# Kernel tuning notes

Measured on AMD Instinct MI355X. Metric: run time of the kernel, lower is better.

## Reference

```python
import jax, jax.numpy as jnp
import numpy as np

Bsz, Hs, Ws, D = 16, 48, 48, 768
N, R, NITERS = 64, 4, 12
NR = N * R


def setup_inputs() -> dict:
    key = jax.random.key(0)
    ks = jax.random.split(key, 16)
    w = lambda k, shape, s=0.02: jax.random.normal(k, shape, jnp.float32) * s
    return {
        "x": jax.random.normal(ks[0], (Bsz, Hs, Ws, D), jnp.float32),
        "W_B": w(ks[1], (D, NR)), "b_B": jnp.zeros((NR,), jnp.float32),
        "W_C": w(ks[2], (D, NR)), "b_C": jnp.zeros((NR,), jnp.float32),
        "W_X": w(ks[3], (D, R)), "b_X": jnp.zeros((R,), jnp.float32),
        "W_dec": w(ks[4], (D, N)), "b_dec": jnp.zeros((N,), jnp.float32),
        "W_th": w(ks[5], (D, N // 2)), "b_th": jnp.zeros((N // 2,), jnp.float32),
        "W_lam": w(ks[6], (D, 1)), "b_lam": jnp.zeros((1,), jnp.float32),
        "B_bias": jnp.ones((NR,), jnp.float32),
        "C_bias": jnp.ones((NR,), jnp.float32),
        "conv_w": w(ks[7], (3, 3, 1, N), 0.1),  # HWIO, depthwise (groups=N)
        "conv_b": jnp.zeros((N,), jnp.float32),
        "W_out": w(ks[8], (NR, D)), "b_out": jnp.zeros((D,), jnp.float32),
    }


def _rope(v, th):
    # v: [B,R,H,W,N], th: [B,H,W,N/2] (broadcast over R). Interleaved pairs.
    c = jnp.cos(th)[:, None]
    s = jnp.sin(th)[:, None]
    vr = v.reshape(v.shape[:-1] + (v.shape[-1] // 2, 2))
    v1, v2 = vr[..., 0], vr[..., 1]
    return jnp.stack([v1 * c - v2 * s, v1 * s + v2 * c], axis=-1).reshape(v.shape)


def reference(x, W_B, b_B, W_C, b_C, W_X, b_X, W_dec, b_dec, W_th, b_th,
              W_lam, b_lam, B_bias, C_bias, conv_w, conv_b, W_out, b_out):
    silu = jax.nn.silu
    Bb, Hh, Ww = x.shape[0], x.shape[1], x.shape[2]

    # Input-dependent (iteration-invariant) projections
    B_proj = silu(x @ W_B + b_B + B_bias).reshape(Bb, Hh, Ww, N, R)
    C_proj = silu(x @ W_C + b_C + C_bias).reshape(Bb, Hh, Ww, N, R)
    B_base = jnp.transpose(B_proj, (0, 4, 1, 2, 3))  # [B,R,H,W,N]
    C_base = jnp.transpose(C_proj, (0, 4, 1, 2, 3))
    Xb = jnp.transpose(silu(x @ W_X + b_X), (0, 3, 1, 2))[..., None]  # [B,R,H,W,1]
    alpha = jax.nn.sigmoid(x @ W_dec + b_dec)[:, None]  # [B,1,H,W,N]
    theta = x @ W_th + b_th                              # [B,H,W,N/2]
    gamma = jax.nn.sigmoid(x @ W_lam + b_lam)[:, None]  # [B,1,H,W,1]

    def diffuse(Hst):
        hf = Hst.reshape(Bb * R, Hh, Ww, N)
        y = jax.lax.conv_general_dilated(
            hf, conv_w, (1, 1), 'SAME',
            dimension_numbers=('NHWC', 'HWIO', 'NHWC'),
            feature_group_count=N) + conv_b
        return y.reshape(Bb, R, Hh, Ww, N)

    Hst = jnp.zeros((Bb, R, Hh, Ww, N), x.dtype)
    prev = None
    for i in range(NITERS):
        inj = _rope(B_base, theta * (i + 1)) * Xb
        Hst = diffuse(Hst)
        if prev is None:
            Hst = alpha * Hst + inj
        else:
            Hst = alpha * Hst + (1.0 - gamma) * alpha * prev + gamma * inj
        prev = inj

    C_rot = _rope(C_base, theta * NITERS)  # layer_idx = n_iters-1 -> scale n_iters
    Hg = C_rot * Hst                        # [B,R,H,W,N]
    Ho = jnp.transpose(Hg, (0, 2, 3, 1, 4)).reshape(Bb, Hh, Ww, R * N)
    return silu(Ho @ W_out + b_out)
```

## Files before the change

kernel.cpp:

```cpp
#include <hip/hip_runtime.h>
#include <hip/hip_bf16.h>
#include <math.h>

#define PTOT 36864
#define DIM 768
#define NCOLS 640
#define IMG 2304
#define KSTEPS 24
#define NPBLK 288

typedef unsigned short ushort_t;
typedef unsigned int uint_t;
typedef __attribute__((ext_vector_type(8))) short bfx8;
typedef __attribute__((ext_vector_type(4))) float f32x4;

#define MFMA_BF16(a, b, c) __builtin_amdgcn_mfma_f32_16x16x32_bf16((a), (b), (c), 0, 0, 0)

__device__ __forceinline__ float sigmoidf_(float v) { return 1.f / (1.f + __expf(-v)); }
__device__ __forceinline__ float siluf_(float v)    { return v   / (1.f + __expf(-v)); }
__device__ __forceinline__ float rfl(float v) {
  return __int_as_float(__builtin_amdgcn_readfirstlane(__float_as_int(v)));
}
__device__ __forceinline__ float bf2f(ushort_t h) {
  return __uint_as_float(((uint_t)h) << 16);
}

typedef __attribute__((address_space(3))) unsigned int lds_uint;
typedef __attribute__((address_space(1))) const unsigned int g_uint;
__device__ __forceinline__ void glds16(const void* gsrc, void* ldst) {
  __builtin_amdgcn_global_load_lds((g_uint*)gsrc, (lds_uint*)ldst, 16, 0, 0);
}

__device__ __forceinline__ void split2(float a, float b, uint_t& hw, uint_t& lw) {
  __hip_bfloat162 hh = __float22bfloat162_rn(make_float2(a, b));
  uint_t hu; __builtin_memcpy(&hu, &hh, 4);
  float ha = __uint_as_float(hu << 16);
  float hb = __uint_as_float(hu & 0xffff0000u);
  __hip_bfloat162 ll = __float22bfloat162_rn(make_float2(a - ha, b - hb));
  uint_t lu; __builtin_memcpy(&lu, &ll, 4);
  hw = hu; lw = lu;
}
__device__ __forceinline__ uint_t cvt2_hi(float a, float b) {
  __hip_bfloat162 hh = __float22bfloat162_rn(make_float2(a, b));
  uint_t hu; __builtin_memcpy(&hu, &hh, 4);
  return hu;
}
__device__ __forceinline__ ushort_t f2bf(float a) {
  return (ushort_t)(cvt2_hi(a, 0.f) & 0xffffu);
}
__device__ __forceinline__ void split8_fast(const float* f, uint4& hi, uint4& lo) {
  uint_t* Hp = (uint_t*)&hi;
  uint_t* Lp = (uint_t*)&lo;
#pragma unroll
  for (int q = 0; q < 4; ++q) split2(f[2 * q], f[2 * q + 1], Hp[q], Lp[q]);
}
__device__ __forceinline__ void cvt8_hi(const float* f, uint4& hi) {
  uint_t* Hp = (uint_t*)&hi;
#pragma unroll
  for (int q = 0; q < 4; ++q) Hp[q] = cvt2_hi(f[2 * q], f[2 * q + 1]);
}

__global__ void pack_kernel(
    const float* __restrict__ W_B, const float* __restrict__ W_C,
    const float* __restrict__ W_dec, const float* __restrict__ W_th,
    const float* __restrict__ W_X, const float* __restrict__ W_lam,
    const float* __restrict__ b_B, const float* __restrict__ b_C,
    const float* __restrict__ b_dec, const float* __restrict__ b_th,
    const float* __restrict__ b_X, const float* __restrict__ b_lam,
    const float* __restrict__ B_bias, const float* __restrict__ C_bias,
    const float* __restrict__ W_out,
    ushort_t* __restrict__ WhiT, ushort_t* __restrict__ WloT,
    ushort_t* __restrict__ WoT, float* __restrict__ bias_all) {
  int idx = blockIdx.x * 256 + threadIdx.x;
  const int NW = NCOLS * DIM;
  const int NWO = DIM * 256;
  if (idx < NW) {
    int c = idx / DIM, k = idx - c * DIM;
    float v;
    if      (c < 256) v = W_B[k * 256 + c];
    else if (c < 512) v = W_C[k * 256 + (c - 256)];
    else if (c < 576) v = W_dec[k * 64 + (c - 512)];
    else if (c < 608) v = W_th[k * 32 + (c - 576)];
    else if (c < 612) v = W_X[k * 4 + (c - 608)];
    else if (c == 612) v = W_lam[k];
    else v = 0.f;
    uint_t hw, lw;
    split2(v, 0.f, hw, lw);
    WhiT[idx] = (ushort_t)(hw & 0xffffu);
    WloT[idx] = (ushort_t)(lw & 0xffffu);
  } else if (idx < NW + NWO) {
    int t = idx - NW;
    int j = t / 256, k = t - j * 256;
    WoT[t] = f2bf(W_out[k * DIM + j]);
  }
  if (idx < NCOLS) {
    int c = idx;
    float v;
    if      (c < 256) v = b_B[c] + B_bias[c];
    else if (c < 512) v = b_C[c - 256] + C_bias[c - 256];
    else if (c < 576) v = b_dec[c - 512];
    else if (c < 608) v = b_th[c - 576];
    else if (c < 612) v = b_X[c - 608];
    else if (c == 612) v = b_lam[0];
    else v = 0.f;
    bias_all[c] = v;
  }
}

template <int HEAVY>
__global__ __launch_bounds__(512, HEAVY ? 4 : 6) void gemm_proj_glds(
    const float* __restrict__ x, const ushort_t* __restrict__ WhiT,
    const ushort_t* __restrict__ WloT, const float* __restrict__ biasall,
    ushort_t* __restrict__ projBC, float* __restrict__ projS) {
  __shared__ ushort_t Ash[2][4096];
  __shared__ ushort_t Asl[HEAVY ? 2 : 1][HEAVY ? 4096 : 4];
  __shared__ float    Bsf[2][4096];
  const int tid = threadIdx.x;
  const int lane = tid & 63, wv = tid >> 6;
  const int wr = wv >> 2, wc = wv & 3;
  const int lk = lane >> 4, lm = lane & 15;

  int cblk, pblk;
  if (HEAVY) {
    int lin = blockIdx.x;
    int id2 = (lin & 7) * 36 + (lin >> 3);
    cblk = 4; pblk = id2;
  } else {
    int lin = blockIdx.x;
    int id2 = (lin & 7) * 144 + (lin >> 3);
    cblk = id2 & 3; pblk = id2 >> 2;
  }
  const int c0 = cblk * 128, p0 = pblk * 128;

  f32x4 acc[4][2];
#pragma unroll
  for (int i = 0; i < 4; ++i)
#pragma unroll
    for (int j = 0; j < 2; ++j) acc[i][j] = (f32x4)0.f;

  auto stage = [&](int buf, int kidx) {
    const int k0 = kidx * 32;
    {
      int mb = __builtin_amdgcn_readfirstlane(wv * 64);
      int m = mb + lane;
      int row = m >> 2, sp = m & 3;
      int g = sp ^ ((row >> 1) & 3);
      glds16(&WhiT[(size_t)(c0 + row) * DIM + k0 + g * 8],
             (void*)&Ash[buf][mb * 8]);
    }
    if (HEAVY) {
      int mb = __builtin_amdgcn_readfirstlane(wv * 64);
      int m = mb + lane;
      int row = m >> 2, sp = m & 3;
      int g = sp ^ ((row >> 1) & 3);
      glds16(&WloT[(size_t)(c0 + row) * DIM + k0 + g * 8],
             (void*)&Asl[buf][mb * 8]);
    }
#pragma unroll
    for (int j = 0; j < 2; ++j) {
      int mb = __builtin_amdgcn_readfirstlane(j * 512 + wv * 64);
      int m = mb + lane;
      int row = m >> 3, sp = m & 7;
      int g = sp ^ (row & 7);
      glds16(&x[(size_t)(p0 + row) * DIM + k0 + g * 4],
             (void*)&Bsf[buf][mb * 4]);
    }
  };

  stage(0, 0);
  __syncthreads();

  for (int kidx = 0; kidx < KSTEPS; ++kidx) {
    const int cur = kidx & 1;
    if (kidx + 1 < KSTEPS) stage(cur ^ 1, kidx + 1);

    bfx8 ah[4], al[4];
#pragma unroll
    for (int f = 0; f < 4; ++f) {
      int row = wr * 64 + f * 16 + lm;
      int sp = lk ^ ((row >> 1) & 3);
      int idx = (row * 4 + sp) * 8;
      ah[f] = *(const bfx8*)&Ash[cur][idx];
      if (HEAVY) al[f] = *(const bfx8*)&Asl[cur][idx];
    }
    bfx8 bh[2], bl[2];
#pragma unroll
    for (int n = 0; n < 2; ++n) {
      int row = wc * 32 + n * 16 + lm;
      int sp0 = (2 * lk)     ^ (row & 7);
      int sp1 = (2 * lk + 1) ^ (row & 7);
      float fv[8];
      *(float4*)&fv[0] = *(const float4*)&Bsf[cur][(row * 8 + sp0) * 4];
      *(float4*)&fv[4] = *(const float4*)&Bsf[cur][(row * 8 + sp1) * 4];
      if (HEAVY) {
        uint4 hv, lv;
        split8_fast(fv, hv, lv);
        bh[n] = *(bfx8*)&hv;
        bl[n] = *(bfx8*)&lv;
      } else {
        uint4 hv;
        cvt8_hi(fv, hv);
        bh[n] = *(bfx8*)&hv;
      }
    }
#pragma unroll
    for (int i = 0; i < 4; ++i)
#pragma unroll
      for (int j = 0; j < 2; ++j) {
        acc[i][j] = MFMA_BF16(ah[i], bh[j], acc[i][j]);
        if (HEAVY) {
          acc[i][j] = MFMA_BF16(al[i], bh[j], acc[i][j]);
          acc[i][j] = MFMA_BF16(ah[i], bl[j], acc[i][j]);
        }
      }
    __syncthreads();
  }

#pragma unroll
  for (int i = 0; i < 4; ++i) {
#pragma unroll
    for (int r = 0; r < 4; ++r) {
      int c = c0 + wr * 64 + i * 16 + lk * 4 + r;
      float bia = biasall[c];
      if (HEAVY) {
        if (c >= 613) continue;
        int rowo = c - 512;
        bool do_silu = (c >= 608 && c < 612);
        bool do_sig  = (c < 576) || (c == 612);
#pragma unroll
        for (int j = 0; j < 2; ++j) {
          float z = acc[i][j][r] + bia;
          if (do_silu) z = siluf_(z);
          else if (do_sig) z = sigmoidf_(z);
          projS[(size_t)rowo * PTOT + p0 + wc * 32 + j * 16 + lm] = z;
        }
      } else {
#pragma unroll
        for (int j = 0; j < 2; ++j) {
          float z = siluf_(acc[i][j][r] + bia);
          projBC[(size_t)c * PTOT + p0 + wc * 32 + j * 16 + lm] = f2bf(z);
        }
      }
    }
  }
}

__global__ __launch_bounds__(256) void iter_kernel(
    const ushort_t* __restrict__ projBC, const float* __restrict__ projS,
    const float* __restrict__ conv_w, const float* __restrict__ conv_b,
    ushort_t* __restrict__ HgBf) {
  const int n2 = blockIdx.x;
  const int r  = blockIdx.y;
  const int b  = blockIdx.z;
  const int n0 = 2 * n2, n1 = n0 + 1;
  const int tid = threadIdx.x;
  const int bh = tid >> 4, bw = tid & 15;
  const int pbase = b * IMG;

  __shared__ float2 HS[2][50 * 51];

  float w0[9], w1[9];
#pragma unroll
  for (int t = 0; t < 9; ++t) {
    w0[t] = rfl(conv_w[t * 64 + n0]);
    w1[t] = rfl(conv_w[t * 64 + n1]);
  }
  const float cvb0 = rfl(conv_b[n0]), cvb1 = rfl(conv_b[n1]);

  {
    float4 zz = {0.f, 0.f, 0.f, 0.f};
    float4* z = (float4*)&HS[0][0];
#pragma unroll
    for (int u = 0; u < 10; ++u) {
      int q = tid + 256 * u;
      if (q < 2550) z[q] = zz;
    }
  }

  const ushort_t* rowB0 = projBC + (size_t)(n0 * 4 + r) * PTOT + pbase;
  const ushort_t* rowB1 = projBC + (size_t)(n1 * 4 + r) * PTOT + pbase;
  const ushort_t* rowC0 = projBC + (size_t)(256 + n0 * 4 + r) * PTOT + pbase;
  const ushort_t* rowC1 = projBC + (size_t)(256 + n1 * 4 + r) * PTOT + pbase;
  const float* rowA0 = projS + (size_t)n0 * PTOT + pbase;
  const float* rowA1 = projS + (size_t)n1 * PTOT + pbase;
  const float* rowTh = projS + (size_t)(64 + n2) * PTOT + pbase;
  const float* rowXv = projS + (size_t)(96 + r) * PTOT + pbase;
  const float* rowGm = projS + (size_t)100 * PTOT + pbase;

  float be0[9], be1[9], cb[9], sb[9], al0[9], al1[9], gmv[9];
#pragma unroll
  for (int s = 0; s < 9; ++s) {
    int dy = s / 3, dx = s - 3 * dy;
    int i = (3 * bh + dy) * 48 + 3 * bw + dx;
    float sn, cn;
    __sincosf(rowTh[i], &sn, &cn);
    cb[s] = cn; sb[s] = sn;
    float B0 = bf2f(rowB0[i]), B1 = bf2f(rowB1[i]), X = rowXv[i];
    be0[s] = (B0 * cn - B1 * sn) * X;
    be1[s] = (B0 * sn + B1 * cn) * X;
    al0[s] = rowA0[i]; al1[s] = rowA1[i];
    gmv[s] = rowGm[i];
  }
  __syncthreads();

  int cur = 0;
  for (int it = 0; it < 12; ++it) {
    float a0[9], a1[9];
#pragma unroll
    for (int s = 0; s < 9; ++s) { a0[s] = cvb0; a1[s] = cvb1; }
#pragma unroll
    for (int yy = 0; yy < 5; ++yy) {
      float2 row[5];
#pragma unroll
      for (int xx = 0; xx < 5; ++xx)
        row[xx] = HS[cur][(3 * bh + yy) * 51 + 3 * bw + xx];
#pragma unroll
      for (int dy = 0; dy < 3; ++dy) {
        int ty = yy - dy;
        if (ty < 0 || ty > 2) continue;
#pragma unroll
        for (int dx = 0; dx < 3; ++dx)
#pragma unroll
          for (int tx = 0; tx < 3; ++tx) {
            a0[dy * 3 + dx] += row[dx + tx].x * w0[ty * 3 + tx];
            a1[dy * 3 + dx] += row[dx + tx].y * w1[ty * 3 + tx];
          }
      }
    }
#pragma unroll
    for (int s = 0; s < 9; ++s) {
      int dy = s / 3, dx = s - 3 * dy;
      float h0, h1;
      if (it == 0) {
        h0 = al0[s] * a0[s] + be0[s];
        h1 = al1[s] * a1[s] + be1[s];
      } else {
        float p0 = be0[s] * cb[s] + be1[s] * sb[s];
        float p1 = be1[s] * cb[s] - be0[s] * sb[s];
        float g = gmv[s];
        h0 = al0[s] * (a0[s] + (1.f - g) * p0) + g * be0[s];
        h1 = al1[s] * (a1[s] + (1.f - g) * p1) + g * be1[s];
      }
      float2 hw; hw.x = h0; hw.y = h1;
      HS[cur ^ 1][(3 * bh + dy + 1) * 51 + (3 * bw + dx + 1)] = hw;
      if (it < 11) {
        float nb0 = be0[s] * cb[s] - be1[s] * sb[s];
        float nb1 = be0[s] * sb[s] + be1[s] * cb[s];
        be0[s] = nb0; be1[s] = nb1;
      }
    }
    __syncthreads();
    cur ^= 1;
  }

  ushort_t* outRow0 = HgBf + (size_t)(r * 64 + n0) * PTOT + pbase;
  ushort_t* outRow1 = HgBf + (size_t)(r * 64 + n1) * PTOT + pbase;
#pragma unroll
  for (int s = 0; s < 9; ++s) {
    int dy = s / 3, dx = s - 3 * dy;
    int i = (3 * bh + dy) * 48 + 3 * bw + dx;
    float c2 = cb[s] * cb[s] - sb[s] * sb[s], s2 = 2.f * cb[s] * sb[s];
    float c4 = c2 * c2 - s2 * s2,             s4 = 2.f * c2 * s2;
    float c8 = c4 * c4 - s4 * s4,             s8 = 2.f * c4 * s4;
    float c12 = c8 * c4 - s8 * s4,            s12 = c8 * s4 + s8 * c4;
    float C0 = bf2f(rowC0[i]), C1 = bf2f(rowC1[i]);
    float cr0 = C0 * c12 - C1 * s12;
    float cr1 = C0 * s12 + C1 * c12;
    float2 hv = HS[cur][(3 * bh + dy + 1) * 51 + (3 * bw + dx + 1)];
    outRow0[i] = f2bf(cr0 * hv.x);
    outRow1[i] = f2bf(cr1 * hv.y);
  }
}

__global__ __launch_bounds__(256) void transpose_cvt(
    const ushort_t* __restrict__ HgBf, ushort_t* __restrict__ Hbf) {
  __shared__ float T[64][65];
  const int tid = threadIdx.x;
  const int p0 = blockIdx.x * 64;
  const int k0 = blockIdx.y * 64;
  {
    int row = tid >> 2, q = tid & 3;
    const ushort_t* src = &HgBf[(size_t)(k0 + row) * PTOT + p0 + q * 16];
    uint4 u0 = *(const uint4*)src;
    uint4 u1 = *(const uint4*)(src + 8);
    const uint_t* up = (const uint_t*)&u0;
#pragma unroll
    for (int t = 0; t < 4; ++t) {
      T[row][q * 16 + 2 * t]     = bf2f((ushort_t)(up[t] & 0xffffu));
      T[row][q * 16 + 2 * t + 1] = bf2f((ushort_t)(up[t] >> 16));
    }
    const uint_t* vp = (const uint_t*)&u1;
#pragma unroll
    for (int t = 0; t < 4; ++t) {
      T[row][q * 16 + 8 + 2 * t]     = bf2f((ushort_t)(vp[t] & 0xffffu));
      T[row][q * 16 + 8 + 2 * t + 1] = bf2f((ushort_t)(vp[t] >> 16));
    }
  }
  __syncthreads();
  {
    int pr = tid >> 2, kq = tid & 3;
    uint_t Hw[8];
#pragma unroll
    for (int q = 0; q < 8; ++q)
      Hw[q] = cvt2_hi(T[kq * 16 + 2 * q][pr], T[kq * 16 + 2 * q + 1][pr]);
    size_t off = (size_t)(p0 + pr) * 256 + k0 + kq * 16;
    *(uint4*)&Hbf[off]     = make_uint4(Hw[0], Hw[1], Hw[2], Hw[3]);
    *(uint4*)&Hbf[off + 8] = make_uint4(Hw[4], Hw[5], Hw[6], Hw[7]);
  }
}

__global__ __launch_bounds__(512, 6) void gemm_out_glds(
    const ushort_t* __restrict__ Hbf, const ushort_t* __restrict__ WoT,
    const float* __restrict__ b_out, float* __restrict__ out) {
  __shared__ ushort_t As[2][4096];
  __shared__ ushort_t Bs[2][4096];
  const int tid = threadIdx.x;
  const int lane = tid & 63, wv = tid >> 6;
  const int wr = wv >> 2, wc = wv & 3;
  const int lk = lane >> 4, lm = lane & 15;
  int lin = blockIdx.x;
  int id2 = (lin & 7) * 216 + (lin >> 3);
  const int jblk = id2 % 6, pblk = id2 / 6;
  const int j0 = jblk * 128, p0 = pblk * 128;

  f32x4 acc[4][2];
#pragma unroll
  for (int i = 0; i < 4; ++i)
#pragma unroll
    for (int j = 0; j < 2; ++j) acc[i][j] = (f32x4)0.f;

  auto stage = [&](int buf, int kidx) {
    const int k0 = kidx * 32;
    {
      int mb = __builtin_amdgcn_readfirstlane(wv * 64);
      int m = mb + lane;
      int row = m >> 2, sp = m & 3;
      int g = sp ^ ((row >> 1) & 3);
      glds16(&Hbf[(size_t)(p0 + row) * 256 + k0 + g * 8],
             (void*)&As[buf][mb * 8]);
    }
    {
      int mb = __builtin_amdgcn_readfirstlane(wv * 64);
      int m = mb + lane;
      int row = m >> 2, sp = m & 3;
      int g = sp ^ ((row >> 1) & 3);
      glds16(&WoT[(size_t)(j0 + row) * 256 + k0 + g * 8],
             (void*)&Bs[buf][mb * 8]);
    }
  };

  stage(0, 0);
  __syncthreads();

  for (int kidx = 0; kidx < 8; ++kidx) {
    const int cur = kidx & 1;
    if (kidx + 1 < 8) stage(cur ^ 1, kidx + 1);
    bfx8 ah[4], bh[2];
#pragma unroll
    for (int f = 0; f < 4; ++f) {
      int ra = wr * 64 + f * 16 + lm;
      int sa = lk ^ ((ra >> 1) & 3);
      ah[f] = *(const bfx8*)&As[cur][(ra * 4 + sa) * 8];
    }
#pragma unroll
    for (int n = 0; n < 2; ++n) {
      int rb = wc * 32 + n * 16 + lm;
      int sb2 = lk ^ ((rb >> 1) & 3);
      bh[n] = *(const bfx8*)&Bs[cur][(rb * 4 + sb2) * 8];
    }
#pragma unroll
    for (int i = 0; i < 4; ++i)
#pragma unroll
      for (int j = 0; j < 2; ++j)
        acc[i][j] = MFMA_BF16(ah[i], bh[j], acc[i][j]);
    __syncthreads();
  }

  float bo[2];
#pragma unroll
  for (int jj = 0; jj < 2; ++jj) bo[jj] = b_out[j0 + wc * 32 + jj * 16 + lm];
#pragma unroll
  for (int i = 0; i < 4; ++i) {
#pragma unroll
    for (int r = 0; r < 4; ++r) {
      int p = p0 + wr * 64 + i * 16 + lk * 4 + r;
      size_t rowoff = (size_t)p * DIM;
#pragma unroll
      for (int jj = 0; jj < 2; ++jj) {
        out[rowoff + j0 + wc * 32 + jj * 16 + lm] =
            siluf_(acc[i][jj][r] + bo[jj]);
      }
    }
  }
}

extern "C" void kernel_launch(void* const* d_in, const int* in_sizes, int n_in,
                              void* d_out, int out_size, void* d_ws, size_t ws_size,
                              hipStream_t stream) {
  const float* x      = (const float*)d_in[0];
  const float* W_B    = (const float*)d_in[1];
  const float* b_B    = (const float*)d_in[2];
  const float* W_C    = (const float*)d_in[3];
  const float* b_C    = (const float*)d_in[4];
  const float* W_X    = (const float*)d_in[5];
  const float* b_X    = (const float*)d_in[6];
  const float* W_dec  = (const float*)d_in[7];
  const float* b_dec  = (const float*)d_in[8];
  const float* W_th   = (const float*)d_in[9];
  const float* b_th   = (const float*)d_in[10];
  const float* W_lam  = (const float*)d_in[11];
  const float* b_lam  = (const float*)d_in[12];
  const float* B_bias = (const float*)d_in[13];
  const float* C_bias = (const float*)d_in[14];
  const float* conv_w = (const float*)d_in[15];
  const float* conv_b = (const float*)d_in[16];
  const float* W_out  = (const float*)d_in[17];
  const float* b_out  = (const float*)d_in[18];
  float* out = (float*)d_out;

  ushort_t* WhiT   = (ushort_t*)d_ws;
  ushort_t* WloT   = WhiT + (size_t)NCOLS * DIM;
  ushort_t* WoT    = WloT + (size_t)NCOLS * DIM;
  float* bias_all  = (float*)(WoT + (size_t)DIM * 256);
  ushort_t* projBC = (ushort_t*)(bias_all + NCOLS);
  float* projS     = (float*)(projBC + (size_t)512 * PTOT);
  ushort_t* HgBf   = (ushort_t*)(projS + (size_t)104 * PTOT);
  ushort_t* Hbf    = HgBf + (size_t)256 * PTOT;

  const int pack_elems = NCOLS * DIM + DIM * 256;
  pack_kernel<<<(pack_elems + 255) / 256, 256, 0, stream>>>(
      W_B, W_C, W_dec, W_th, W_X, W_lam,
      b_B, b_C, b_dec, b_th, b_X, b_lam, B_bias, C_bias, W_out,
      WhiT, WloT, WoT, bias_all);

  gemm_proj_glds<0><<<dim3(4 * NPBLK), 512, 0, stream>>>(
      x, WhiT, WloT, bias_all, projBC, projS);
  gemm_proj_glds<1><<<dim3(NPBLK), 512, 0, stream>>>(
      x, WhiT, WloT, bias_all, projBC, projS);

  iter_kernel<<<dim3(32, 4, 16), 256, 0, stream>>>(
      projBC, projS, conv_w, conv_b, HgBf);

  transpose_cvt<<<dim3(PTOT / 64, 4), 256, 0, stream>>>(HgBf, Hbf);

  gemm_out_glds<<<dim3(6 * NPBLK), 512, 0, stream>>>(
      Hbf, WoT, b_out, out);
}
```

Measured before the change: 244.1 us.

## Load GEMM operands directly from global memory into registers, bypassing LDS

The light projection GEMM (B/C columns) and the output GEMM drop LDS double-buffering and barriers. Each wave now loads its MFMA fragments straight from global memory into registers. The heavy split-precision projection path is split into its own non-templated kernel and keeps its LDS staging. This removes LDS traffic and __syncthreads, but gives up operand sharing across waves, so global/L2 traffic rises and there is no software prefetch to hide load latency.

Result: slower. 440.5 us (+80.5%).

```diff
diff --git a/kernel.cpp b/kernel.cpp
--- a/kernel.cpp
+++ b/kernel.cpp
@@ -107,29 +107,82 @@
   }
 }
 
-template <int HEAVY>
-__global__ __launch_bounds__(512, HEAVY ? 4 : 6) void gemm_proj_glds(
+__global__ __launch_bounds__(512, 6) void gemm_proj_direct(
+    const float* __restrict__ x, const ushort_t* __restrict__ WhiT,
+    const float* __restrict__ biasall, ushort_t* __restrict__ projBC) {
+  const int tid = threadIdx.x;
+  const int lane = tid & 63, wv = tid >> 6;
+  const int wr = wv >> 2, wc = wv & 3;
+  const int lk = lane >> 4, lm = lane & 15;
+
+  int lin = blockIdx.x;
+  int id2 = (lin & 7) * 144 + (lin >> 3);
+  const int cblk = id2 & 3, pblk = id2 >> 2;
+  const int c0 = cblk * 128, p0 = pblk * 128;
+
+  const ushort_t* wbase = WhiT + (size_t)(c0 + wr * 64 + lm) * DIM + lk * 8;
+  const float*    xbase = x    + (size_t)(p0 + wc * 32 + lm) * DIM + lk * 8;
+
+  f32x4 acc[4][2];
+#pragma unroll
+  for (int i = 0; i < 4; ++i)
+#pragma unroll
+    for (int j = 0; j < 2; ++j) acc[i][j] = (f32x4)0.f;
+
+  for (int kidx = 0; kidx < KSTEPS; ++kidx) {
+    const int k0 = kidx * 32;
+    bfx8 ah[4];
+#pragma unroll
+    for (int f = 0; f < 4; ++f)
+      ah[f] = *(const bfx8*)(wbase + (size_t)f * 16 * DIM + k0);
+    bfx8 bh[2];
+#pragma unroll
+    for (int n = 0; n < 2; ++n) {
+      const float* xq = xbase + (size_t)n * 16 * DIM + k0;
+      float fv[8];
+      *(float4*)&fv[0] = *(const float4*)xq;
+      *(float4*)&fv[4] = *(const float4*)(xq + 4);
+      uint4 hv;
+      cvt8_hi(fv, hv);
+      bh[n] = *(bfx8*)&hv;
+    }
+#pragma unroll
+    for (int i = 0; i < 4; ++i)
+#pragma unroll
+      for (int j = 0; j < 2; ++j)
+        acc[i][j] = MFMA_BF16(ah[i], bh[j], acc[i][j]);
+  }
+
+#pragma unroll
+  for (int i = 0; i < 4; ++i) {
+#pragma unroll
+    for (int r = 0; r < 4; ++r) {
+      int c = c0 + wr * 64 + i * 16 + lk * 4 + r;
+      float bia = biasall[c];
+#pragma unroll
+      for (int j = 0; j < 2; ++j) {
+        float z = siluf_(acc[i][j][r] + bia);
+        projBC[(size_t)c * PTOT + p0 + wc * 32 + j * 16 + lm] = f2bf(z);
+      }
+    }
+  }
+}
+
+__global__ __launch_bounds__(512, 4) void gemm_proj_heavy(
     const float* __restrict__ x, const ushort_t* __restrict__ WhiT,
     const ushort_t* __restrict__ WloT, const float* __restrict__ biasall,
-    ushort_t* __restrict__ projBC, float* __restrict__ projS) {
+    float* __restrict__ projS) {
   __shared__ ushort_t Ash[2][4096];
-  __shared__ ushort_t Asl[HEAVY ? 2 : 1][HEAVY ? 4096 : 4];
+  __shared__ ushort_t Asl[2][4096];
   __shared__ float    Bsf[2][4096];
   const int tid = threadIdx.x;
   const int lane = tid & 63, wv = tid >> 6;
   const int wr = wv >> 2, wc = wv & 3;
   const int lk = lane >> 4, lm = lane & 15;
 
-  int cblk, pblk;
-  if (HEAVY) {
-    int lin = blockIdx.x;
-    int id2 = (lin & 7) * 36 + (lin >> 3);
-    cblk = 4; pblk = id2;
-  } else {
-    int lin = blockIdx.x;
-    int id2 = (lin & 7) * 144 + (lin >> 3);
-    cblk = id2 & 3; pblk = id2 >> 2;
-  }
+  int lin = blockIdx.x;
+  int id2 = (lin & 7) * 36 + (lin >> 3);
+  const int cblk = 4, pblk = id2;
   const int c0 = cblk * 128, p0 = pblk * 128;
 
   f32x4 acc[4][2];
@@ -148,7 +201,7 @@
       glds16(&WhiT[(size_t)(c0 + row) * DIM + k0 + g * 8],
              (void*)&Ash[buf][mb * 8]);
     }
-    if (HEAVY) {
+    {
       int mb = __builtin_amdgcn_readfirstlane(wv * 64);
       int m = mb + lane;
       int row = m >> 2, sp = m & 3;
@@ -181,7 +234,7 @@
       int sp = lk ^ ((row >> 1) & 3);
       int idx = (row * 4 + sp) * 8;
       ah[f] = *(const bfx8*)&Ash[cur][idx];
-      if (HEAVY) al[f] = *(const bfx8*)&Asl[cur][idx];
+      al[f] = *(const bfx8*)&Asl[cur][idx];
     }
     bfx8 bh[2], bl[2];
 #pragma unroll
@@ -192,26 +245,18 @@
       float fv[8];
       *(float4*)&fv[0] = *(const float4*)&Bsf[cur][(row * 8 + sp0) * 4];
       *(float4*)&fv[4] = *(const float4*)&Bsf[cur][(row * 8 + sp1) * 4];
-      if (HEAVY) {
-        uint4 hv, lv;
-        split8_fast(fv, hv, lv);
-        bh[n] = *(bfx8*)&hv;
-        bl[n] = *(bfx8*)&lv;
-      } else {
-        uint4 hv;
-        cvt8_hi(fv, hv);
-        bh[n] = *(bfx8*)&hv;
-      }
+      uint4 hv, lv;
+      split8_fast(fv, hv, lv);
+      bh[n] = *(bfx8*)&hv;
+      bl[n] = *(bfx8*)&lv;
     }
 #pragma unroll
     for (int i = 0; i < 4; ++i)
 #pragma unroll
       for (int j = 0; j < 2; ++j) {
         acc[i][j] = MFMA_BF16(ah[i], bh[j], acc[i][j]);
-        if (HEAVY) {
-          acc[i][j] = MFMA_BF16(al[i], bh[j], acc[i][j]);
-          acc[i][j] = MFMA_BF16(ah[i], bl[j], acc[i][j]);
-        }
+        acc[i][j] = MFMA_BF16(al[i], bh[j], acc[i][j]);
+        acc[i][j] = MFMA_BF16(ah[i], bl[j], acc[i][j]);
       }
     __syncthreads();
   }
@@ -221,25 +266,17 @@
 #pragma unroll
     for (int r = 0; r < 4; ++r) {
       int c = c0 + wr * 64 + i * 16 + lk * 4 + r;
+      if (c >= 613) continue;
       float bia = biasall[c];
-      if (HEAVY) {
-        if (c >= 613) continue;
-        int rowo = c - 512;
-        bool do_silu = (c >= 608 && c < 612);
-        bool do_sig  = (c < 576) || (c == 612);
-#pragma unroll
-        for (int j = 0; j < 2; ++j) {
-          float z = acc[i][j][r] + bia;
-          if (do_silu) z = siluf_(z);
-          else if (do_sig) z = sigmoidf_(z);
-          projS[(size_t)rowo * PTOT + p0 + wc * 32 + j * 16 + lm] = z;
-        }
-      } else {
-#pragma unroll
-        for (int j = 0; j < 2; ++j) {
-          float z = siluf_(acc[i][j][r] + bia);
-          projBC[(size_t)c * PTOT + p0 + wc * 32 + j * 16 + lm] = f2bf(z);
-        }
+      int rowo = c - 512;
+      bool do_silu = (c >= 608 && c < 612);
+      bool do_sig  = (c < 576) || (c == 612);
+#pragma unroll
+      for (int j = 0; j < 2; ++j) {
+        float z = acc[i][j][r] + bia;
+        if (do_silu) z = siluf_(z);
+        else if (do_sig) z = sigmoidf_(z);
+        projS[(size_t)rowo * PTOT + p0 + wc * 32 + j * 16 + lm] = z;
       }
     }
   }
@@ -409,11 +446,9 @@
   }
 }
 
-__global__ __launch_bounds__(512, 6) void gemm_out_glds(
+__global__ __launch_bounds__(512, 6) void gemm_out_direct(
     const ushort_t* __restrict__ Hbf, const ushort_t* __restrict__ WoT,
     const float* __restrict__ b_out, float* __restrict__ out) {
-  __shared__ ushort_t As[2][4096];
-  __shared__ ushort_t Bs[2][4096];
   const int tid = threadIdx.x;
   const int lane = tid & 63, wv = tid >> 6;
   const int wr = wv >> 2, wc = wv & 3;
@@ -423,57 +458,30 @@
   const int jblk = id2 % 6, pblk = id2 / 6;
   const int j0 = jblk * 128, p0 = pblk * 128;
 
+  const ushort_t* abase = Hbf + (size_t)(p0 + wr * 64 + lm) * 256 + lk * 8;
+  const ushort_t* bbase = WoT + (size_t)(j0 + wc * 32 + lm) * 256 + lk * 8;
+
   f32x4 acc[4][2];
 #pragma unroll
   for (int i = 0; i < 4; ++i)
 #pragma unroll
     for (int j = 0; j < 2; ++j) acc[i][j] = (f32x4)0.f;
 
-  auto stage = [&](int buf, int kidx) {
+  for (int kidx = 0; kidx < 8; ++kidx) {
     const int k0 = kidx * 32;
-    {
-      int mb = __builtin_amdgcn_readfirstlane(wv * 64);
-      int m = mb + lane;
-      int row = m >> 2, sp = m & 3;
-      int g = sp ^ ((row >> 1) & 3);
-      glds16(&Hbf[(size_t)(p0 + row) * 256 + k0 + g * 8],
-             (void*)&As[buf][mb * 8]);
-    }
-    {
-      int mb = __builtin_amdgcn_readfirstlane(wv * 64);
-      int m = mb + lane;
-      int row = m >> 2, sp = m & 3;
-      int g = sp ^ ((row >> 1) & 3);
-      glds16(&WoT[(size_t)(j0 + row) * 256 + k0 + g * 8],
-             (void*)&Bs[buf][mb * 8]);
-    }
-  };
-
-  stage(0, 0);
-  __syncthreads();
-
-  for (int kidx = 0; kidx < 8; ++kidx) {
-    const int cur = kidx & 1;
-    if (kidx + 1 < 8) stage(cur ^ 1, kidx + 1);
-    bfx8 ah[4], bh[2];
-#pragma unroll
-    for (int f = 0; f < 4; ++f) {
-      int ra = wr * 64 + f * 16 + lm;
-      int sa = lk ^ ((ra >> 1) & 3);
-      ah[f] = *(const bfx8*)&As[cur][(ra * 4 + sa) * 8];
-    }
-#pragma unroll
-    for (int n = 0; n < 2; ++n) {
-      int rb = wc * 32 + n * 16 + lm;
-      int sb2 = lk ^ ((rb >> 1) & 3);
-      bh[n] = *(const bfx8*)&Bs[cur][(rb * 4 + sb2) * 8];
-    }
+    bfx8 ah[4];
+#pragma unroll
+    for (int f = 0; f < 4; ++f)
+      ah[f] = *(const bfx8*)(abase + (size_t)f * 16 * 256 + k0);
+    bfx8 bh[2];
+#pragma unroll
+    for (int n = 0; n < 2; ++n)
+      bh[n] = *(const bfx8*)(bbase + (size_t)n * 16 * 256 + k0);
 #pragma unroll
     for (int i = 0; i < 4; ++i)
 #pragma unroll
       for (int j = 0; j < 2; ++j)
         acc[i][j] = MFMA_BF16(ah[i], bh[j], acc[i][j]);
-    __syncthreads();
   }
 
   float bo[2];
@@ -533,16 +541,16 @@
       b_B, b_C, b_dec, b_th, b_X, b_lam, B_bias, C_bias, W_out,
       WhiT, WloT, WoT, bias_all);
 
-  gemm_proj_glds<0><<<dim3(4 * NPBLK), 512, 0, stream>>>(
-      x, WhiT, WloT, bias_all, projBC, projS);
-  gemm_proj_glds<1><<<dim3(NPBLK), 512, 0, stream>>>(
-      x, WhiT, WloT, bias_all, projBC, projS);
+  gemm_proj_direct<<<dim3(4 * NPBLK), 512, 0, stream>>>(
+      x, WhiT, bias_all, projBC);
+  gemm_proj_heavy<<<dim3(NPBLK), 512, 0, stream>>>(
+      x, WhiT, WloT, bias_all, projS);
 
   iter_kernel<<<dim3(32, 4, 16), 256, 0, stream>>>(
       projBC, projS, conv_w, conv_b, HgBf);
 
   transpose_cvt<<<dim3(PTOT / 64, 4), 256, 0, stream>>>(HgBf, Hbf);
 
-  gemm_out_glds<<<dim3(6 * NPBLK), 512, 0, stream>>>(
+  gemm_out_direct<<<dim3(6 * NPBLK), 512, 0, stream>>>(
       Hbf, WoT, b_out, out);
 }
```
